# Performance work log

Measured on AMD Instinct MI355X. Metric: run time of the kernel, lower is better.

The kernel has to match this reference:

```python
import jax, jax.numpy as jnp
import numpy as np

EPS = 0.0  # init_eps=0, learn_eps=False -> fixed buffer
N_NODES = 50000
N_EDGES = 800000
D_NODE = 128
D_EDGE = 64


def setup_inputs() -> dict:
    key = jax.random.key(0)
    ks = jax.random.split(key, 10)
    s = lambda fan: 1.0 / np.sqrt(fan)
    return {
        "node_feat": jax.random.normal(ks[0], (N_NODES, D_NODE), jnp.float32),
        "edge_feat": jax.random.normal(ks[1], (N_EDGES, D_EDGE), jnp.float32),
        "W0": jax.random.normal(ks[2], (D_EDGE, D_EDGE), jnp.float32) * s(D_EDGE),
        "b0": jax.random.normal(ks[3], (D_EDGE,), jnp.float32) * s(D_EDGE),
        "W1": jax.random.normal(ks[4], (D_EDGE, D_NODE), jnp.float32) * s(D_EDGE),
        "b1": jax.random.normal(ks[5], (D_NODE,), jnp.float32) * s(D_EDGE),
        "Wa": jax.random.normal(ks[6], (D_NODE, D_NODE), jnp.float32) * s(D_NODE),
        "ba": jax.random.normal(ks[7], (D_NODE,), jnp.float32) * s(D_NODE),
        "src": jax.random.randint(ks[8], (N_EDGES,), 0, N_NODES, jnp.int64),
        "dst": jax.random.randint(ks[9], (N_EDGES,), 0, N_NODES, jnp.int64),
    }


def reference(node_feat, edge_feat, W0, b0, W1, b1, Wa, ba, src, dst):
    # edge transform MLP: relu(Linear) -> relu(Linear)  [E, D_NODE]
    e = jax.nn.relu(edge_feat @ W0 + b0)
    e = jax.nn.relu(e @ W1 + b1)
    # per-edge message: relu(x_src + e)  [E, D_NODE]
    m = jax.nn.relu(node_feat[src] + e)
    # scatter-sum to destination nodes  [N, D_NODE]
    neigh = jax.ops.segment_sum(m, dst, num_segments=node_feat.shape[0])
    rst = (1.0 + EPS) * node_feat + neigh
    # apply_func: Linear(128, 128)
    return rst @ Wa + ba
```

## Files before the change

### kernel.cpp

```cpp
#include <hip/hip_runtime.h>

typedef short bf16x8 __attribute__((ext_vector_type(8)));
typedef float f32x4 __attribute__((ext_vector_type(4)));
typedef unsigned short u16x4 __attribute__((ext_vector_type(4)));
typedef unsigned short u16x8 __attribute__((ext_vector_type(8)));

static constexpr int N_NODES = 50000;
static constexpr int N_EDGES = 800000;
static constexpr int D_NODE = 128;
static constexpr int D_EDGE = 64;

static constexpr size_t START_OFF = 0;
static constexpr size_t FILL_OFF  = 262144;
static constexpr size_t POS_OFF   = 524288;
static constexpr size_t MSG_OFF   = POS_OFF + (size_t)N_EDGES * 4;
static constexpr size_t WS_NEED   = MSG_OFF + (size_t)N_EDGES * D_NODE * 2;

__device__ __forceinline__ unsigned short f2bf(float f) {
    union { float f; unsigned u; } v; v.f = f;
    return (unsigned short)((v.u + 0x7fffu + ((v.u >> 16) & 1u)) >> 16);
}
__device__ __forceinline__ float bf2f(unsigned short h) {
    union { unsigned u; float f; } v; v.u = ((unsigned)h) << 16;
    return v.f;
}

__global__ void kz(int* __restrict__ a, int n) {
    int i = blockIdx.x * blockDim.x + threadIdx.x;
    if (i < n) a[i] = 0;
}

__global__ void kh(const int* __restrict__ dst, int* __restrict__ start) {
    int e = blockIdx.x * blockDim.x + threadIdx.x;
    if (e < N_EDGES) atomicAdd(&start[dst[e] + 1], 1);
}

__global__ __launch_bounds__(256) void ks1(const int* __restrict__ a, int* __restrict__ bsum, int n) {
    __shared__ int sd[256];
    const int t = threadIdx.x;
    int i = blockIdx.x * 256 + t;
    sd[t] = (i < n) ? a[i] : 0;
    __syncthreads();
    for (int off = 128; off > 0; off >>= 1) {
        if (t < off) sd[t] += sd[t + off];
        __syncthreads();
    }
    if (t == 0) bsum[blockIdx.x] = sd[0];
}

__global__ __launch_bounds__(256) void ks2(int* __restrict__ bsum, int nb) {
    __shared__ int sd[256];
    const int t = threadIdx.x;
    sd[t] = (t < nb) ? bsum[t] : 0;
    __syncthreads();
    for (int off = 1; off < 256; off <<= 1) {
        int v = (t >= off) ? sd[t - off] : 0;
        __syncthreads();
        sd[t] += v;
        __syncthreads();
    }
    if (t < nb) bsum[t] = sd[t];
}

__global__ __launch_bounds__(256) void ks3(const int* __restrict__ bsum,
                                           int* __restrict__ start, int* __restrict__ fill, int n) {
    __shared__ int sd[256];
    const int t = threadIdx.x;
    const int i = blockIdx.x * 256 + t;
    sd[t] = (i < n) ? start[i] : 0;
    __syncthreads();
    for (int off = 1; off < 256; off <<= 1) {
        int v = (t >= off) ? sd[t - off] : 0;
        __syncthreads();
        sd[t] += v;
        __syncthreads();
    }
    const int off0 = (blockIdx.x > 0) ? bsum[blockIdx.x - 1] : 0;
    const int val = sd[t] + off0;
    if (i < n) start[i] = val;
    if (i < N_NODES) fill[i] = val;
}

__global__ void kpos(const int* __restrict__ dst, int* __restrict__ fill, int* __restrict__ pos) {
    int e = blockIdx.x * blockDim.x + threadIdx.x;
    if (e < N_EDGES) pos[e] = atomicAdd(&fill[dst[e]], 1);
}

__global__ __launch_bounds__(256) void k_edge_msg(
    const float* __restrict__ ef, const float* __restrict__ nf,
    const float* __restrict__ W0, const float* __restrict__ b0,
    const float* __restrict__ W1, const float* __restrict__ b1,
    const int* __restrict__ src, const int* __restrict__ posp,
    unsigned short* __restrict__ msg)
{
    __shared__ unsigned short w0f[2 * 4 * 64 * 8];
    __shared__ unsigned short w1f[2 * 8 * 64 * 8];
    __shared__ __align__(16) unsigned short hT[4][16][72];
    __shared__ __align__(16) unsigned short mT[4][16][136];

    const int tid = threadIdx.x;
    for (int f = tid; f < 4096; f += 256) {
        int j = f & 7, lane = (f >> 3) & 63, nt = (f >> 9) & 3, ks = (f >> 11) & 1;
        int k = ks * 32 + ((lane >> 4) << 2) + (j & 3) + ((j & 4) << 2);
        int n = nt * 16 + (lane & 15);
        w0f[f] = f2bf(W0[k * 64 + n]);
    }
    for (int f = tid; f < 8192; f += 256) {
        int j = f & 7, lane = (f >> 3) & 63, nt = (f >> 9) & 7, ks = (f >> 12) & 1;
        int k = ks * 32 + ((lane >> 4) << 2) + (j & 3) + ((j & 4) << 2);
        int n = nt * 16 + (lane & 15);
        w1f[f] = f2bf(W1[k * 128 + n]);
    }
    __syncthreads();

    const int wv = tid >> 6;
    const int lane = tid & 63;
    const int lm = lane & 15;
    const int lq = lane >> 4;

    float b0r[4], b1r[8];
#pragma unroll
    for (int nt = 0; nt < 4; ++nt) b0r[nt] = b0[nt * 16 + lm];
#pragma unroll
    for (int nt = 0; nt < 8; ++nt) b1r[nt] = b1[nt * 16 + lm];

    const bf16x8* w0v = (const bf16x8*)w0f;
    const bf16x8* w1v = (const bf16x8*)w1f;

    const int wtile0 = (blockIdx.x * 4 + wv) * 4;

    int sidx[4][4], pidx[4][4];
#pragma unroll
    for (int t = 0; t < 4; ++t) {
        const int ebase = (wtile0 + t) * 16;
#pragma unroll
        for (int r = 0; r < 4; ++r) sidx[t][r] = src[ebase + lq * 4 + r];
#pragma unroll
        for (int p = 0; p < 4; ++p) pidx[t][p] = posp[ebase + p * 4 + lq];
    }

    for (int t = 0; t < 4; ++t) {
        const int ebase = (wtile0 + t) * 16;

        const f32x4* er = (const f32x4*)(ef + (size_t)(ebase + lm) * D_EDGE);
        f32x4 a0 = er[lq];
        f32x4 a1 = er[4 + lq];
        f32x4 a2 = er[8 + lq];
        f32x4 a3 = er[12 + lq];

        float ng[4][8];
#pragma unroll
        for (int r = 0; r < 4; ++r) {
            const float* nrow = nf + (size_t)sidx[t][r] * D_NODE;
#pragma unroll
            for (int nt = 0; nt < 8; ++nt) ng[r][nt] = nrow[nt * 16 + lm];
        }

        bf16x8 af0, af1;
#pragma unroll
        for (int j = 0; j < 4; ++j) {
            af0[j] = (short)f2bf(a0[j]); af0[j + 4] = (short)f2bf(a1[j]);
            af1[j] = (short)f2bf(a2[j]); af1[j + 4] = (short)f2bf(a3[j]);
        }

        f32x4 h[4];
#pragma unroll
        for (int nt = 0; nt < 4; ++nt) h[nt] = f32x4{0.f, 0.f, 0.f, 0.f};
#pragma unroll
        for (int nt = 0; nt < 4; ++nt) {
            h[nt] = __builtin_amdgcn_mfma_f32_16x16x32_bf16(af0, w0v[(0 * 4 + nt) * 64 + lane], h[nt], 0, 0, 0);
            h[nt] = __builtin_amdgcn_mfma_f32_16x16x32_bf16(af1, w0v[(1 * 4 + nt) * 64 + lane], h[nt], 0, 0, 0);
        }
#pragma unroll
        for (int nt = 0; nt < 4; ++nt)
#pragma unroll
            for (int r = 0; r < 4; ++r) {
                float x = h[nt][r] + b0r[nt];
                hT[wv][lq * 4 + r][nt * 16 + lm] = f2bf(fmaxf(x, 0.f));
            }

        const unsigned short* hrow = &hT[wv][lm][0];
        u16x4 p0 = *(const u16x4*)(hrow + lq * 4);
        u16x4 p1 = *(const u16x4*)(hrow + 16 + lq * 4);
        u16x4 p2 = *(const u16x4*)(hrow + 32 + lq * 4);
        u16x4 p3 = *(const u16x4*)(hrow + 48 + lq * 4);
        bf16x8 g0, g1;
#pragma unroll
        for (int j = 0; j < 4; ++j) {
            g0[j] = (short)p0[j]; g0[j + 4] = (short)p1[j];
            g1[j] = (short)p2[j]; g1[j + 4] = (short)p3[j];
        }

        f32x4 o[8];
#pragma unroll
        for (int nt = 0; nt < 8; ++nt) o[nt] = f32x4{0.f, 0.f, 0.f, 0.f};
#pragma unroll
        for (int nt = 0; nt < 8; ++nt) {
            o[nt] = __builtin_amdgcn_mfma_f32_16x16x32_bf16(g0, w1v[(0 * 8 + nt) * 64 + lane], o[nt], 0, 0, 0);
            o[nt] = __builtin_amdgcn_mfma_f32_16x16x32_bf16(g1, w1v[(1 * 8 + nt) * 64 + lane], o[nt], 0, 0, 0);
        }

#pragma unroll
        for (int r = 0; r < 4; ++r)
#pragma unroll
            for (int nt = 0; nt < 8; ++nt) {
                float e2 = fmaxf(o[nt][r] + b1r[nt], 0.f);
                float x = e2 + ng[r][nt];
                mT[wv][lq * 4 + r][nt * 16 + lm] = f2bf(fmaxf(x, 0.f));
            }

#pragma unroll
        for (int p = 0; p < 4; ++p) {
            const int row = p * 4 + lq;
            u16x8 v = *(const u16x8*)&mT[wv][row][lm * 8];
            *(u16x8*)(msg + (size_t)pidx[t][p] * D_NODE + lm * 8) = v;
        }
    }
}

__global__ __launch_bounds__(256) void k_reduce(
    const float* __restrict__ nf, const unsigned short* __restrict__ msg,
    const int* __restrict__ start, float* __restrict__ out)
{
    const int tid = threadIdx.x;
    const int wv = tid >> 6;
    const int lane = tid & 63;
    const int lq = lane >> 4;
    const int li = lane & 15;
    const int v = blockIdx.x * 4 + wv;
    if (v >= N_NODES) return;

    const int s = start[v];
    const int e = start[v + 1];

    f32x4 acc0 = f32x4{0.f, 0.f, 0.f, 0.f};
    f32x4 acc1 = f32x4{0.f, 0.f, 0.f, 0.f};

    for (int i = s + lq; i < e; i += 4) {
        u16x8 m = *(const u16x8*)(msg + (size_t)i * D_NODE + li * 8);
#pragma unroll
        for (int j = 0; j < 4; ++j) acc0[j] += bf2f(m[j]);
#pragma unroll
        for (int j = 0; j < 4; ++j) acc1[j] += bf2f(m[4 + j]);
    }

#pragma unroll
    for (int j = 0; j < 4; ++j) {
        acc0[j] += __shfl_xor(acc0[j], 16);
        acc0[j] += __shfl_xor(acc0[j], 32);
        acc1[j] += __shfl_xor(acc1[j], 16);
        acc1[j] += __shfl_xor(acc1[j], 32);
    }

    if (lq == 0) {
        const f32x4* nrow = (const f32x4*)(nf + (size_t)v * D_NODE);
        f32x4* orow = (f32x4*)(out + (size_t)v * D_NODE);
        orow[li * 2] = nrow[li * 2] + acc0;
        orow[li * 2 + 1] = nrow[li * 2 + 1] + acc1;
    }
}

__global__ void k_copy(const f32x4* __restrict__ s, f32x4* __restrict__ d, int n4) {
    int stride = gridDim.x * blockDim.x;
    for (int i = blockIdx.x * blockDim.x + threadIdx.x; i < n4; i += stride)
        d[i] = s[i];
}

__global__ __launch_bounds__(256) void k_edge(
    const float* __restrict__ ef, const float* __restrict__ nf,
    const float* __restrict__ W0, const float* __restrict__ b0,
    const float* __restrict__ W1, const float* __restrict__ b1,
    const int* __restrict__ src, const int* __restrict__ dst,
    float* __restrict__ acc)
{
    __shared__ unsigned short w0f[2 * 4 * 64 * 8];
    __shared__ unsigned short w1f[2 * 8 * 64 * 8];
    __shared__ unsigned short hT[4][16][72];

    const int tid = threadIdx.x;
    for (int f = tid; f < 4096; f += 256) {
        int j = f & 7, lane = (f >> 3) & 63, nt = (f >> 9) & 3, ks = (f >> 11) & 1;
        int k = ks * 32 + ((lane >> 4) << 2) + (j & 3) + ((j & 4) << 2);
        int n = nt * 16 + (lane & 15);
        w0f[f] = f2bf(W0[k * 64 + n]);
    }
    for (int f = tid; f < 8192; f += 256) {
        int j = f & 7, lane = (f >> 3) & 63, nt = (f >> 9) & 7, ks = (f >> 12) & 1;
        int k = ks * 32 + ((lane >> 4) << 2) + (j & 3) + ((j & 4) << 2);
        int n = nt * 16 + (lane & 15);
        w1f[f] = f2bf(W1[k * 128 + n]);
    }
    __syncthreads();

    const int wv = tid >> 6;
    const int lane = tid & 63;
    const int lm = lane & 15;
    const int lq = lane >> 4;

    float b0r[4], b1r[8];
#pragma unroll
    for (int nt = 0; nt < 4; ++nt) b0r[nt] = b0[nt * 16 + lm];
#pragma unroll
    for (int nt = 0; nt < 8; ++nt) b1r[nt] = b1[nt * 16 + lm];

    const bf16x8* w0v = (const bf16x8*)w0f;
    const bf16x8* w1v = (const bf16x8*)w1f;

    for (int t = 0; t < 4; ++t) {
        const int tile = (blockIdx.x * 4 + wv) * 4 + t;
        const int ebase = tile * 16;

        const f32x4* er = (const f32x4*)(ef + (size_t)(ebase + lm) * D_EDGE);
        f32x4 a0 = er[lq];
        f32x4 a1 = er[4 + lq];
        f32x4 a2 = er[8 + lq];
        f32x4 a3 = er[12 + lq];
        bf16x8 af0, af1;
#pragma unroll
        for (int j = 0; j < 4; ++j) {
            af0[j] = (short)f2bf(a0[j]); af0[j + 4] = (short)f2bf(a1[j]);
            af1[j] = (short)f2bf(a2[j]); af1[j + 4] = (short)f2bf(a3[j]);
        }

        f32x4 h[4];
#pragma unroll
        for (int nt = 0; nt < 4; ++nt) h[nt] = f32x4{0.f, 0.f, 0.f, 0.f};
#pragma unroll
        for (int nt = 0; nt < 4; ++nt) {
            h[nt] = __builtin_amdgcn_mfma_f32_16x16x32_bf16(af0, w0v[(0 * 4 + nt) * 64 + lane], h[nt], 0, 0, 0);
            h[nt] = __builtin_amdgcn_mfma_f32_16x16x32_bf16(af1, w0v[(1 * 4 + nt) * 64 + lane], h[nt], 0, 0, 0);
        }
#pragma unroll
        for (int nt = 0; nt < 4; ++nt)
#pragma unroll
            for (int r = 0; r < 4; ++r) {
                float x = h[nt][r] + b0r[nt];
                hT[wv][lq * 4 + r][nt * 16 + lm] = f2bf(fmaxf(x, 0.f));
            }

        const unsigned short* hrow = &hT[wv][lm][0];
        u16x4 p0 = *(const u16x4*)(hrow + lq * 4);
        u16x4 p1 = *(const u16x4*)(hrow + 16 + lq * 4);
        u16x4 p2 = *(const u16x4*)(hrow + 32 + lq * 4);
        u16x4 p3 = *(const u16x4*)(hrow + 48 + lq * 4);
        bf16x8 g0, g1;
#pragma unroll
        for (int j = 0; j < 4; ++j) {
            g0[j] = (short)p0[j]; g0[j + 4] = (short)p1[j];
            g1[j] = (short)p2[j]; g1[j + 4] = (short)p3[j];
        }

        f32x4 o[8];
#pragma unroll
        for (int nt = 0; nt < 8; ++nt) o[nt] = f32x4{0.f, 0.f, 0.f, 0.f};
#pragma unroll
        for (int nt = 0; nt < 8; ++nt) {
            o[nt] = __builtin_amdgcn_mfma_f32_16x16x32_bf16(g0, w1v[(0 * 8 + nt) * 64 + lane], o[nt], 0, 0, 0);
            o[nt] = __builtin_amdgcn_mfma_f32_16x16x32_bf16(g1, w1v[(1 * 8 + nt) * 64 + lane], o[nt], 0, 0, 0);
        }

        const int e0 = ebase + lq * 4;
        int s_[4], d_[4];
#pragma unroll
        for (int r = 0; r < 4; ++r) { s_[r] = src[e0 + r]; d_[r] = dst[e0 + r]; }
#pragma unroll
        for (int r = 0; r < 4; ++r) {
            const float* nrow = nf + (size_t)s_[r] * D_NODE;
            float* arow = acc + (size_t)d_[r] * D_NODE;
#pragma unroll
            for (int nt = 0; nt < 8; ++nt) {
                float e2 = fmaxf(o[nt][r] + b1r[nt], 0.f);
                float x = e2 + nrow[nt * 16 + lm];
                unsafeAtomicAdd(&arow[nt * 16 + lm], fmaxf(x, 0.f));
            }
        }
    }
}

__global__ __launch_bounds__(256) void k_out(
    const float* __restrict__ Wa, const float* __restrict__ ba,
    float* __restrict__ out)
{
    __shared__ unsigned short waf[4 * 8 * 64 * 8];

    const int tid = threadIdx.x;
    for (int f = tid; f < 16384; f += 256) {
        int j = f & 7, lane = (f >> 3) & 63, nt = (f >> 9) & 7, ks = (f >> 12) & 3;
        int k = ks * 32 + ((lane >> 4) << 2) + (j & 3) + ((j & 4) << 2);
        int n = nt * 16 + (lane & 15);
        waf[f] = f2bf(Wa[k * 128 + n]);
    }
    __syncthreads();

    const int wv = tid >> 6;
    const int lane = tid & 63;
    const int lm = lane & 15;
    const int lq = lane >> 4;

    const int tile = blockIdx.x * 4 + wv;
    if (tile >= N_NODES / 16) return;
    const int rbase = tile * 16;

    const f32x4* arow = (const f32x4*)(out + (size_t)(rbase + lm) * D_NODE);
    const bf16x8* wav = (const bf16x8*)waf;

    bf16x8 afr[4];
#pragma unroll
    for (int ks = 0; ks < 4; ++ks) {
        f32x4 y0 = arow[ks * 8 + lq];
        f32x4 y1 = arow[ks * 8 + 4 + lq];
#pragma unroll
        for (int j = 0; j < 4; ++j) {
            afr[ks][j] = (short)f2bf(y0[j]);
            afr[ks][j + 4] = (short)f2bf(y1[j]);
        }
    }

    float bar[8];
#pragma unroll
    for (int nt = 0; nt < 8; ++nt) bar[nt] = ba[nt * 16 + lm];

    f32x4 o[8];
#pragma unroll
    for (int nt = 0; nt < 8; ++nt) o[nt] = f32x4{0.f, 0.f, 0.f, 0.f};
#pragma unroll
    for (int ks = 0; ks < 4; ++ks)
#pragma unroll
        for (int nt = 0; nt < 8; ++nt)
            o[nt] = __builtin_amdgcn_mfma_f32_16x16x32_bf16(afr[ks], wav[(ks * 8 + nt) * 64 + lane], o[nt], 0, 0, 0);

#pragma unroll
    for (int nt = 0; nt < 8; ++nt)
#pragma unroll
        for (int r = 0; r < 4; ++r)
            out[(size_t)(rbase + lq * 4 + r) * D_NODE + nt * 16 + lm] = o[nt][r] + bar[nt];
}

extern "C" void kernel_launch(void* const* d_in, const int* in_sizes, int n_in,
                              void* d_out, int out_size, void* d_ws, size_t ws_size,
                              hipStream_t stream) {
    const float* nf = (const float*)d_in[0];
    const float* ef = (const float*)d_in[1];
    const float* W0 = (const float*)d_in[2];
    const float* b0 = (const float*)d_in[3];
    const float* W1 = (const float*)d_in[4];
    const float* b1 = (const float*)d_in[5];
    const float* Wa = (const float*)d_in[6];
    const float* ba = (const float*)d_in[7];
    const int* src = (const int*)d_in[8];
    const int* dst = (const int*)d_in[9];
    float* out = (float*)d_out;

    if (ws_size >= WS_NEED) {
        char* ws = (char*)d_ws;
        int* start = (int*)(ws + START_OFF);
        int* fill  = (int*)(ws + FILL_OFF);
        int* pos   = (int*)(ws + POS_OFF);
        int* bsum  = pos;
        unsigned short* msg = (unsigned short*)(ws + MSG_OFF);

        const int n_scan = N_NODES + 1;
        const int nb = (n_scan + 255) / 256;

        kz<<<(n_scan + 255) / 256, 256, 0, stream>>>(start, n_scan);
        kh<<<(N_EDGES + 255) / 256, 256, 0, stream>>>(dst, start);
        ks1<<<nb, 256, 0, stream>>>(start, bsum, n_scan);
        ks2<<<1, 256, 0, stream>>>(bsum, nb);
        ks3<<<nb, 256, 0, stream>>>(bsum, start, fill, n_scan);
        kpos<<<(N_EDGES + 255) / 256, 256, 0, stream>>>(dst, fill, pos);

        k_edge_msg<<<N_EDGES / (16 * 4 * 4), 256, 0, stream>>>(
            ef, nf, W0, b0, W1, b1, src, pos, msg);
        k_reduce<<<(N_NODES + 3) / 4, 256, 0, stream>>>(nf, msg, start, out);
    } else {
        k_copy<<<2048, 256, 0, stream>>>((const f32x4*)nf, (f32x4*)out, N_NODES * D_NODE / 4);
        k_edge<<<N_EDGES / (16 * 4 * 4), 256, 0, stream>>>(ef, nf, W0, b0, W1, b1, src, dst, out);
    }

    k_out<<<(N_NODES / 16 + 3) / 4, 256, 0, stream>>>(Wa, ba, out);
}
```

Baseline: 303.0 us.

## Fuse edge MLP with dst-sorted segmented atomic scatter, drop message buffer

Replaces the scheme that wrote bf16 messages to a dst-sorted buffer and then reduced them per node. The counting-sort pass now emits a permutation plus permuted src/dst arrays. The edge kernel processes edges in dst-sorted order, gathers edge features through the permutation, and pre-reduces runs of equal dst within each 16-edge tile before issuing float atomics into the output. This removes the 200MB message write and read and the separate reduce kernel. In exchange it adds random gathers of edge_feat rows, atomic traffic, and an extra __syncthreads inside the tile loop.

```diff
diff --git a/kernel.cpp b/kernel.cpp
--- a/kernel.cpp
+++ b/kernel.cpp
@@ -2,6 +2,7 @@
 
 typedef short bf16x8 __attribute__((ext_vector_type(8)));
 typedef float f32x4 __attribute__((ext_vector_type(4)));
+typedef unsigned short u16x2 __attribute__((ext_vector_type(2)));
 typedef unsigned short u16x4 __attribute__((ext_vector_type(4)));
 typedef unsigned short u16x8 __attribute__((ext_vector_type(8)));
 
@@ -12,9 +13,10 @@
 
 static constexpr size_t START_OFF = 0;
 static constexpr size_t FILL_OFF  = 262144;
-static constexpr size_t POS_OFF   = 524288;
-static constexpr size_t MSG_OFF   = POS_OFF + (size_t)N_EDGES * 4;
-static constexpr size_t WS_NEED   = MSG_OFF + (size_t)N_EDGES * D_NODE * 2;
+static constexpr size_t PERM_OFF  = 524288;
+static constexpr size_t SRCP_OFF  = PERM_OFF + (size_t)N_EDGES * 4;
+static constexpr size_t DSTP_OFF  = SRCP_OFF + (size_t)N_EDGES * 4;
+static constexpr size_t WS_NEED   = DSTP_OFF + (size_t)N_EDGES * 4;
 
 __device__ __forceinline__ unsigned short f2bf(float f) {
     union { float f; unsigned u; } v; v.f = f;
@@ -81,17 +83,25 @@
     if (i < N_NODES) fill[i] = val;
 }
 
-__global__ void kpos(const int* __restrict__ dst, int* __restrict__ fill, int* __restrict__ pos) {
+__global__ void kpos(const int* __restrict__ dst, const int* __restrict__ src,
+                     int* __restrict__ fill, int* __restrict__ perm,
+                     int* __restrict__ srcp, int* __restrict__ dstp) {
     int e = blockIdx.x * blockDim.x + threadIdx.x;
-    if (e < N_EDGES) pos[e] = atomicAdd(&fill[dst[e]], 1);
-}
-
-__global__ __launch_bounds__(256) void k_edge_msg(
+    if (e < N_EDGES) {
+        int d = dst[e];
+        int p = atomicAdd(&fill[d], 1);
+        perm[p] = e;
+        srcp[p] = src[e];
+        dstp[p] = d;
+    }
+}
+
+__global__ __launch_bounds__(256) void k_edge_fused(
     const float* __restrict__ ef, const float* __restrict__ nf,
     const float* __restrict__ W0, const float* __restrict__ b0,
     const float* __restrict__ W1, const float* __restrict__ b1,
-    const int* __restrict__ src, const int* __restrict__ posp,
-    unsigned short* __restrict__ msg)
+    const int* __restrict__ perm, const int* __restrict__ srcp,
+    const int* __restrict__ dstp, float* __restrict__ out)
 {
     __shared__ unsigned short w0f[2 * 4 * 64 * 8];
     __shared__ unsigned short w1f[2 * 8 * 64 * 8];
@@ -129,20 +139,14 @@
 
     const int wtile0 = (blockIdx.x * 4 + wv) * 4;
 
-    int sidx[4][4], pidx[4][4];
-#pragma unroll
     for (int t = 0; t < 4; ++t) {
         const int ebase = (wtile0 + t) * 16;
-#pragma unroll
-        for (int r = 0; r < 4; ++r) sidx[t][r] = src[ebase + lq * 4 + r];
-#pragma unroll
-        for (int p = 0; p < 4; ++p) pidx[t][p] = posp[ebase + p * 4 + lq];
-    }
-
-    for (int t = 0; t < 4; ++t) {
-        const int ebase = (wtile0 + t) * 16;
-
-        const f32x4* er = (const f32x4*)(ef + (size_t)(ebase + lm) * D_EDGE);
+
+        const int e_m = perm[ebase + lm];
+        const int s_m = srcp[ebase + lm];
+        const int d_m = dstp[ebase + lm];
+
+        const f32x4* er = (const f32x4*)(ef + (size_t)e_m * D_EDGE);
         f32x4 a0 = er[lq];
         f32x4 a1 = er[4 + lq];
         f32x4 a2 = er[8 + lq];
@@ -151,7 +155,8 @@
         float ng[4][8];
 #pragma unroll
         for (int r = 0; r < 4; ++r) {
-            const float* nrow = nf + (size_t)sidx[t][r] * D_NODE;
+            const int s_row = __shfl(s_m, lq * 4 + r);
+            const float* nrow = nf + (size_t)s_row * D_NODE;
 #pragma unroll
             for (int nt = 0; nt < 8; ++nt) ng[r][nt] = nrow[nt * 16 + lm];
         }
@@ -209,54 +214,29 @@
                 mT[wv][lq * 4 + r][nt * 16 + lm] = f2bf(fmaxf(x, 0.f));
             }
 
-#pragma unroll
-        for (int p = 0; p < 4; ++p) {
-            const int row = p * 4 + lq;
-            u16x8 v = *(const u16x8*)&mT[wv][row][lm * 8];
-            *(u16x8*)(msg + (size_t)pidx[t][p] * D_NODE + lm * 8) = v;
-        }
-    }
-}
-
-__global__ __launch_bounds__(256) void k_reduce(
-    const float* __restrict__ nf, const unsigned short* __restrict__ msg,
-    const int* __restrict__ start, float* __restrict__ out)
-{
-    const int tid = threadIdx.x;
-    const int wv = tid >> 6;
-    const int lane = tid & 63;
-    const int lq = lane >> 4;
-    const int li = lane & 15;
-    const int v = blockIdx.x * 4 + wv;
-    if (v >= N_NODES) return;
-
-    const int s = start[v];
-    const int e = start[v + 1];
-
-    f32x4 acc0 = f32x4{0.f, 0.f, 0.f, 0.f};
-    f32x4 acc1 = f32x4{0.f, 0.f, 0.f, 0.f};
-
-    for (int i = s + lq; i < e; i += 4) {
-        u16x8 m = *(const u16x8*)(msg + (size_t)i * D_NODE + li * 8);
-#pragma unroll
-        for (int j = 0; j < 4; ++j) acc0[j] += bf2f(m[j]);
-#pragma unroll
-        for (int j = 0; j < 4; ++j) acc1[j] += bf2f(m[4 + j]);
-    }
-
-#pragma unroll
-    for (int j = 0; j < 4; ++j) {
-        acc0[j] += __shfl_xor(acc0[j], 16);
-        acc0[j] += __shfl_xor(acc0[j], 32);
-        acc1[j] += __shfl_xor(acc1[j], 16);
-        acc1[j] += __shfl_xor(acc1[j], 32);
-    }
-
-    if (lq == 0) {
-        const f32x4* nrow = (const f32x4*)(nf + (size_t)v * D_NODE);
-        f32x4* orow = (f32x4*)(out + (size_t)v * D_NODE);
-        orow[li * 2] = nrow[li * 2] + acc0;
-        orow[li * 2 + 1] = nrow[li * 2 + 1] + acc1;
+        asm volatile("" ::: "memory");
+        __syncthreads();
+
+        float acc0 = 0.f, acc1 = 0.f;
+        int dprev = __shfl(d_m, 0);
+#pragma unroll
+        for (int r = 0; r < 16; ++r) {
+            const int dr = __shfl(d_m, r);
+            if (dr != dprev) {
+                float* orow = out + (size_t)dprev * D_NODE + lane * 2;
+                unsafeAtomicAdd(orow, acc0);
+                unsafeAtomicAdd(orow + 1, acc1);
+                acc0 = 0.f; acc1 = 0.f; dprev = dr;
+            }
+            const u16x2 v = *(const u16x2*)&mT[wv][r][lane * 2];
+            acc0 += bf2f(v[0]);
+            acc1 += bf2f(v[1]);
+        }
+        float* orow = out + (size_t)dprev * D_NODE + lane * 2;
+        unsafeAtomicAdd(orow, acc0);
+        unsafeAtomicAdd(orow + 1, acc1);
+
+        asm volatile("" ::: "memory");
     }
 }
 
@@ -451,13 +431,16 @@
     const int* dst = (const int*)d_in[9];
     float* out = (float*)d_out;
 
+    k_copy<<<2048, 256, 0, stream>>>((const f32x4*)nf, (f32x4*)out, N_NODES * D_NODE / 4);
+
     if (ws_size >= WS_NEED) {
         char* ws = (char*)d_ws;
         int* start = (int*)(ws + START_OFF);
         int* fill  = (int*)(ws + FILL_OFF);
-        int* pos   = (int*)(ws + POS_OFF);
-        int* bsum  = pos;
-        unsigned short* msg = (unsigned short*)(ws + MSG_OFF);
+        int* perm  = (int*)(ws + PERM_OFF);
+        int* srcp  = (int*)(ws + SRCP_OFF);
+        int* dstp  = (int*)(ws + DSTP_OFF);
+        int* bsum  = perm;
 
         const int n_scan = N_NODES + 1;
         const int nb = (n_scan + 255) / 256;
@@ -467,13 +450,11 @@
         ks1<<<nb, 256, 0, stream>>>(start, bsum, n_scan);
         ks2<<<1, 256, 0, stream>>>(bsum, nb);
         ks3<<<nb, 256, 0, stream>>>(bsum, start, fill, n_scan);
-        kpos<<<(N_EDGES + 255) / 256, 256, 0, stream>>>(dst, fill, pos);
-
-        k_edge_msg<<<N_EDGES / (16 * 4 * 4), 256, 0, stream>>>(
-            ef, nf, W0, b0, W1, b1, src, pos, msg);
-        k_reduce<<<(N_NODES + 3) / 4, 256, 0, stream>>>(nf, msg, start, out);
+        kpos<<<(N_EDGES + 255) / 256, 256, 0, stream>>>(dst, src, fill, perm, srcp, dstp);
+
+        k_edge_fused<<<N_EDGES / (16 * 4 * 4), 256, 0, stream>>>(
+            ef, nf, W0, b0, W1, b1, perm, srcp, dstp, out);
     } else {
-        k_copy<<<2048, 256, 0, stream>>>((const f32x4*)nf, (f32x4*)out, N_NODES * D_NODE / 4);
         k_edge<<<N_EDGES / (16 * 4 * 4), 256, 0, stream>>>(ef, nf, W0, b0, W1, b1, src, dst, out);
     }
 
```

Result: faster. 290.1 us (-4.2%).
